# Kernel optimization log

Hardware: AMD Instinct MI355X
Metric: run time of the kernel (lower is better)

The kernel has to match this reference:

```python
import jax, jax.numpy as jnp
import numpy as np

JITTER = 1e-6
LOG_2PI_BASE = 2.0 * np.pi  # multiplied by sigma_sq inside log


def rbf_kernel(x1, x2, lengthscale, outputscale):
    """gpytorch ScaleKernel(RBFKernel): outputscale * exp(-0.5 * ||(x1-x2)/ls||^2)."""
    x1s = x1 / lengthscale
    x2s = x2 / lengthscale
    sq = (jnp.sum(x1s * x1s, axis=1)[:, None]
          + jnp.sum(x2s * x2s, axis=1)[None, :]
          - 2.0 * (x1s @ x2s.T))
    sq = jnp.maximum(sq, 0.0)
    return outputscale * jnp.exp(-0.5 * sq)


def setup_inputs() -> dict:
    key = jax.random.key(0)
    k = jax.random.split(key, 4)
    n, m, d = 8192, 512, 8
    return {
        "train_x": jax.random.normal(k[0], (n, d), dtype=jnp.float32),
        "train_y": jax.random.normal(k[1], (n,), dtype=jnp.float32),
        "inducing_points": jax.random.normal(k[2], (m, d), dtype=jnp.float32),
        "q_mu": jnp.zeros((m, 1), dtype=jnp.float32),
        "q_log_var": jnp.eye(m, dtype=jnp.float32),
        "likelihood_log_variance": jnp.asarray(0.0, dtype=jnp.float32),
        "lengthscale": jnp.asarray(1.0, dtype=jnp.float32),
        "outputscale": jnp.asarray(1.0, dtype=jnp.float32),
    }


def reference(train_x, train_y, inducing_points, q_mu, q_log_var,
              likelihood_log_variance, lengthscale, outputscale):
    n = train_x.shape[0]
    m = inducing_points.shape[0]
    eye_m = jnp.eye(m, dtype=train_x.dtype)

    # --- predict(train_x): q(f) = N(pred_mean, pred_cov) ---
    K_ff = rbf_kernel(train_x, train_x, lengthscale, outputscale)          # [n, n]
    K_uu = rbf_kernel(inducing_points, inducing_points, lengthscale, outputscale) + JITTER * eye_m
    K_uf = rbf_kernel(inducing_points, train_x, lengthscale, outputscale)  # [m, n]

    L_uu = jnp.linalg.cholesky(K_uu)                                       # lower [m, m]
    Lam = jax.scipy.linalg.solve_triangular(L_uu, K_uf, lower=True)        # [m, n]
    pred_mean = (Lam.T @ q_mu)[:, 0]                                       # [n]

    q_sqrt = jnp.tril(jnp.exp(0.5 * q_log_var))                            # [m, m]
    q_cov = q_sqrt @ q_sqrt.T + JITTER * eye_m                             # [m, m]

    S = K_ff - Lam.T @ Lam                                                 # [n, n]
    V = Lam.T @ q_cov                                                      # [n, m]
    pred_cov = S + V @ V.T                                                 # [n, n]

    # --- expected log likelihood E_{q(f)}[log N(y | f, sigma^2 I)] / n ---
    sigma_sq = jnp.exp(likelihood_log_variance)
    diff = train_y - pred_mean
    ell = jnp.sum(-0.5 * (diff * diff + jnp.diagonal(pred_cov)) / sigma_sq
                  - 0.5 * jnp.log(LOG_2PI_BASE * sigma_sq)) / n

    # --- KL( N(q_mu, q_cov) || N(0, I) ) / n ---
    Lq = jnp.linalg.cholesky(q_cov)
    logdet_q = 2.0 * jnp.sum(jnp.log(jnp.diagonal(Lq)))
    mu = q_mu[:, 0]
    kl = 0.5 * (jnp.trace(q_cov) + mu @ mu - m - logdet_q) / n

    return ell - kl
```

## Files before the change

### kernel.cpp

```cpp
#include <hip/hip_runtime.h>
#include <math.h>

#define MI 512
#define NPT 8192
#define JIT 1e-6f
#define LOG2PI 1.8378770664093453f

#define OFF_A     0
#define OFF_LINV  262144
#define OFF_QS    524288
#define OFF_QC    786432
#define OFF_DINV  1048576
#define OFF_PART  1081856
#define OFF_FLAGS 1082368
#define NFLAGS 209

#define FMA16(ACC,a0,a1,a2,a3,b0,b1,b2,b3) \
  ACC[0][0]+=a0*b0; ACC[0][1]+=a0*b1; ACC[0][2]+=a0*b2; ACC[0][3]+=a0*b3; \
  ACC[1][0]+=a1*b0; ACC[1][1]+=a1*b1; ACC[1][2]+=a1*b2; ACC[1][3]+=a1*b3; \
  ACC[2][0]+=a2*b0; ACC[2][1]+=a2*b1; ACC[2][2]+=a2*b2; ACC[2][3]+=a2*b3; \
  ACC[3][0]+=a3*b0; ACC[3][1]+=a3*b1; ACC[3][2]+=a3*b2; ACC[3][3]+=a3*b3;

__device__ __forceinline__ void wait_flag(unsigned* f, int tid) {
  if (tid == 0) {
    while (__hip_atomic_load(f, __ATOMIC_RELAXED, __HIP_MEMORY_SCOPE_AGENT) == 0)
      __builtin_amdgcn_s_sleep(2);
    __builtin_amdgcn_fence(__ATOMIC_ACQUIRE, "agent");
  }
  __syncthreads();
}
__device__ __forceinline__ void wait_count(unsigned* c, unsigned tgt, int tid) {
  if (tid == 0) {
    while (__hip_atomic_load(c, __ATOMIC_RELAXED, __HIP_MEMORY_SCOPE_AGENT) < tgt)
      __builtin_amdgcn_s_sleep(2);
    __builtin_amdgcn_fence(__ATOMIC_ACQUIRE, "agent");
  }
  __syncthreads();
}
__device__ __forceinline__ void raise_flag(unsigned* f, int tid) {
  __syncthreads();
  if (tid == 0) {
    __builtin_amdgcn_fence(__ATOMIC_RELEASE, "agent");
    __hip_atomic_store(f, 1u, __ATOMIC_RELAXED, __HIP_MEMORY_SCOPE_AGENT);
  }
}
__device__ __forceinline__ void publish_tile(unsigned* f, unsigned* cnt, int tid) {
  __syncthreads();
  if (tid == 0) {
    __builtin_amdgcn_fence(__ATOMIC_RELEASE, "agent");
    __hip_atomic_store(f, 1u, __ATOMIC_RELAXED, __HIP_MEMORY_SCOPE_AGENT);
    __hip_atomic_fetch_add(cnt, 1u, __ATOMIC_RELAXED, __HIP_MEMORY_SCOPE_AGENT);
  }
}

__global__ __launch_bounds__(256) void k_prep(const float* __restrict__ Z,
    const float* __restrict__ qlv, const float* __restrict__ lsP,
    const float* __restrict__ osP, float* __restrict__ ws) {
  int u = blockIdx.x*256 + threadIdx.x;
  if (blockIdx.x < 27) {
    int fi = blockIdx.x*256 + threadIdx.x;
    if (fi < NFLAGS*32) ((unsigned*)(ws + OFF_FLAGS))[fi] = 0u;
  }
  float ls = lsP[0], os = osP[0];
  float ils2 = 1.0f/(ls*ls);
  if (u < MI*MI) {
    int i = u >> 9, j = u & 511;
    float4 a0 = *(const float4*)(Z + i*8);
    float4 a1 = *(const float4*)(Z + i*8 + 4);
    float4 b0 = *(const float4*)(Z + j*8);
    float4 b1 = *(const float4*)(Z + j*8 + 4);
    float d0=a0.x-b0.x, d1=a0.y-b0.y, d2=a0.z-b0.z, d3=a0.w-b0.w;
    float d4=a1.x-b1.x, d5=a1.y-b1.y, d6=a1.z-b1.z, d7=a1.w-b1.w;
    float sq = d0*d0+d1*d1+d2*d2+d3*d3+d4*d4+d5*d5+d6*d6+d7*d7;
    float v = os*__expf(-0.5f*ils2*sq);
    if (i==j) v += JIT;
    ws[OFF_A + u] = v;
  } else {
    int w2 = u - MI*MI;
    if (w2 < MI*MI) {
      int i = w2 >> 9, j = w2 & 511;
      ws[OFF_QS + w2] = (j <= i) ? __expf(0.5f*qlv[w2]) : 0.0f;
    }
  }
}

__global__ __launch_bounds__(256) void k_gemm_nt(const float* __restrict__ X,
    const float* __restrict__ Y, float* __restrict__ O, float adiag) {
  __shared__ float Xs[64][20], Ys[64][20];
  int tid = threadIdx.x;
  int bi = blockIdx.y, bj = blockIdx.x;
  int ty4 = (tid >> 4)*4, tx4 = (tid & 15)*4;
  int lrow = tid >> 2, lc4 = (tid & 3)*4;
  float acc[4][4] = {{0.f}};
  for (int kc = 0; kc < 512; kc += 16) {
    float4 xa = *(const float4*)(X + (bi*64+lrow)*512 + kc + lc4);
    float4 ya = *(const float4*)(Y + (bj*64+lrow)*512 + kc + lc4);
    Xs[lrow][lc4+0]=xa.x; Xs[lrow][lc4+1]=xa.y; Xs[lrow][lc4+2]=xa.z; Xs[lrow][lc4+3]=xa.w;
    Ys[lrow][lc4+0]=ya.x; Ys[lrow][lc4+1]=ya.y; Ys[lrow][lc4+2]=ya.z; Ys[lrow][lc4+3]=ya.w;
    __syncthreads();
    #pragma unroll
    for (int kk = 0; kk < 16; ++kk) {
      float a0=Xs[ty4+0][kk],a1=Xs[ty4+1][kk],a2=Xs[ty4+2][kk],a3=Xs[ty4+3][kk];
      float b0=Ys[tx4+0][kk],b1=Ys[tx4+1][kk],b2=Ys[tx4+2][kk],b3=Ys[tx4+3][kk];
      FMA16(acc,a0,a1,a2,a3,b0,b1,b2,b3)
    }
    __syncthreads();
  }
  #pragma unroll
  for (int u = 0; u < 4; ++u)
    #pragma unroll
    for (int v = 0; v < 4; ++v) {
      int gi = bi*64+ty4+u, gj = bj*64+tx4+v;
      float o = acc[u][v]; if (gi==gj) o += adiag;
      O[gi*512+gj] = o;
    }
}

__global__ __launch_bounds__(256, 3) void k_dag(const float* __restrict__ X,
    const float* __restrict__ Yv, const float* __restrict__ Z,
    const float* __restrict__ qmu, const float* __restrict__ llvP,
    const float* __restrict__ lsP, const float* __restrict__ osP,
    float* __restrict__ ws) {
  __shared__ float SH[13340];
  float* A    = ws + OFF_A;
  float* LT   = ws + OFF_LINV;
  const float* QC = ws + OFF_QC;
  float* DINV = ws + OFF_DINV;
  float* PART = ws + OFF_PART;
  unsigned* FB = (unsigned*)(ws + OFF_FLAGS);
  #define FLA(i) (FB + (i)*32)
  int bid = blockIdx.x, tid = threadIdx.x;
  int ty4 = (tid >> 4)*4, tx4 = (tid & 15)*4;

  if (bid < 8) {
    __builtin_amdgcn_s_setprio(3);
    int b = bid, Rb = b*64;
    float* Dg = SH;
    float* Sa = SH + 4160;
    float* Sb = SH + 8320;
    float* TMP = SH + 12480;
    for (int e = tid; e < 4096; e += 256)
      Dg[(e>>6)*65 + (e&63)] = A[(Rb + (e>>6))*512 + Rb + (e&63)];

    for (int p = 0; p < b; ++p) {
      if (p > 0) wait_flag(FLA(144 + b*8 + p), tid);
      for (int e = tid; e < 4096; e += 256)
        Sb[(e>>6)*65 + (e&63)] = A[(Rb + (e>>6))*512 + p*64 + (e&63)];
      wait_flag(FLA(p), tid);
      for (int e = tid; e < 4096; e += 256)
        Sa[(e>>6)*65 + (e&63)] = DINV[p*4096 + e];
      __syncthreads();
      float acc2[4][4] = {{0.f}};
      for (int m = 0; m < 64; ++m) {
        float a0=Sb[(ty4+0)*65+m],a1=Sb[(ty4+1)*65+m],a2=Sb[(ty4+2)*65+m],a3=Sb[(ty4+3)*65+m];
        float b0=Sa[(tx4+0)*65+m],b1=Sa[(tx4+1)*65+m],b2=Sa[(tx4+2)*65+m],b3=Sa[(tx4+3)*65+m];
        FMA16(acc2,a0,a1,a2,a3,b0,b1,b2,b3)
      }
      __syncthreads();
      #pragma unroll
      for (int u = 0; u < 4; ++u)
        #pragma unroll
        for (int v = 0; v < 4; ++v) {
          Sb[(ty4+u)*65 + tx4+v] = acc2[u][v];
          A[(Rb+ty4+u)*512 + p*64 + tx4+v] = acc2[u][v];
        }
      raise_flag(FLA(8 + b*8 + p), tid);
      float c2[4][4] = {{0.f}};
      for (int m = 0; m < 64; ++m) {
        float a0=Sb[(ty4+0)*65+m],a1=Sb[(ty4+1)*65+m],a2=Sb[(ty4+2)*65+m],a3=Sb[(ty4+3)*65+m];
        float b0=Sb[(tx4+0)*65+m],b1=Sb[(tx4+1)*65+m],b2=Sb[(tx4+2)*65+m],b3=Sb[(tx4+3)*65+m];
        FMA16(c2,a0,a1,a2,a3,b0,b1,b2,b3)
      }
      #pragma unroll
      for (int u = 0; u < 4; ++u)
        #pragma unroll
        for (int v = 0; v < 4; ++v)
          Dg[(ty4+u)*65 + tx4+v] -= c2[u][v];
    }
    __syncthreads();

    for (int e = tid; e < 4096; e += 256) Sa[(e>>6)*65 + (e&63)] = 0.0f;
    __syncthreads();
    for (int t = 0; t < 4; ++t) {
      const int c0 = t*16;
      if (tid < 16) {
        float a[16];
        #pragma unroll
        for (int j = 0; j < 16; ++j) a[j] = Dg[(c0+tid)*65 + c0 + j];
        float rr = 0.f;
        #pragma unroll
        for (int j = 0; j < 16; ++j) {
          float d = __shfl(a[j], j);
          float r = rsqrtf(d);
          r = r*(1.5f - 0.5f*d*r*r);
          if (tid == j) rr = r;
          a[j] *= r;
          #pragma unroll
          for (int k = j+1; k < 16; ++k)
            a[k] -= a[j]*__shfl(a[j], k);
        }
        #pragma unroll
        for (int j = 0; j < 16; ++j)
          Dg[(c0+tid)*65 + c0 + j] = (j <= tid) ? a[j] : 0.0f;
        float v[16];
        #pragma unroll
        for (int i = 0; i < 16; ++i) {
          float s = (tid == i) ? 1.0f : 0.0f;
          #pragma unroll
          for (int k = 0; k < i; ++k)
            s -= Dg[(c0+i)*65 + c0 + k]*v[k];
          v[i] = s * __shfl(rr, i);
        }
        #pragma unroll
        for (int i = 0; i < 16; ++i)
          Sa[(c0+i)*65 + c0 + tid] = v[i];
      }
      __syncthreads();
      if (t < 3) {
        const int cnt = 48 - c0;
        const int r0 = c0 + 16;
        float res[3];
        int nout = cnt*16, idx = 0;
        for (int e = tid; e < nout; e += 256, ++idx) {
          int r = r0 + (e >> 4), j = e & 15;
          float s = 0.f;
          #pragma unroll
          for (int m = 0; m < 16; ++m)
            s += Dg[r*65 + c0 + m]*Sa[(c0+j)*65 + c0 + m];
          res[idx] = s;
        }
        __syncthreads();
        idx = 0;
        for (int e = tid; e < nout; e += 256, ++idx)
          Dg[(r0 + (e >> 4))*65 + c0 + (e & 15)] = res[idx];
        __syncthreads();
        for (int e = tid; e < cnt*cnt; e += 256) {
          int r = r0 + e/cnt, c = r0 + e%cnt;
          float s = 0.f;
          #pragma unroll
          for (int m = 0; m < 16; ++m)
            s += Dg[r*65 + c0 + m]*Dg[c*65 + c0 + m];
          Dg[r*65 + c] -= s;
        }
        __syncthreads();
      }
    }
    for (int d = 1; d < 4; ++d) {
      int nout = (4-d)*256;
      for (int e = tid; e < nout; e += 256) {
        int bs = e >> 8, I = bs, J = I + d;
        int i = (e >> 4) & 15, c = e & 15;
        float s = 0.f;
        for (int k = I; k < J; ++k) {
          #pragma unroll
          for (int m = 0; m < 16; ++m)
            s += Dg[(J*16+i)*65 + k*16+m]*Sa[(k*16+m)*65 + I*16+c];
        }
        TMP[bs*272 + i*17 + c] = s;
      }
      __syncthreads();
      for (int e = tid; e < nout; e += 256) {
        int bs = e >> 8, I = bs, J = I + d;
        int i = (e >> 4) & 15, c = e & 15;
        float s = 0.f;
        #pragma unroll
        for (int m = 0; m < 16; ++m)
          s += Sa[(J*16+i)*65 + J*16+m]*TMP[bs*272 + m*17 + c];
        Sa[(J*16+i)*65 + I*16+c] = -s;
      }
      __syncthreads();
    }
    for (int e = tid; e < 4096; e += 256)
      DINV[b*4096 + e] = Sa[(e>>6)*65 + (e&63)];
    raise_flag(FLA(b), tid);
    return;
  }

  if (bid < 44) {
    __builtin_amdgcn_s_setprio(2);
    int t = bid - 8;
    int s = 0, rem = t;
    while (rem >= s+1) { rem -= (s+1); ++s; }
    int J = rem;
    if (s == J) {
      wait_flag(FLA(s), tid);
      for (int e = tid; e < 4096; e += 256) {
        int i = e >> 6, j = e & 63;
        LT[(64*s+j)*512 + 64*s + i] = DINV[s*4096 + e];
      }
      publish_tile(FLA(72 + s*8 + J), FLA(136 + s), tid);
      return;
    }
    float* Ls = SH;
    float* Vs = SH + 4160;
    float* T  = SH + 8320;
    float acc[4][4] = {{0.f}};
    for (int k = J; k < s; ++k) {
      wait_flag(FLA(72 + k*8 + J), tid);
      wait_flag(FLA(8 + s*8 + k), tid);
      for (int e = tid; e < 1024; e += 256) {
        int row = e >> 4, m4 = (e & 15)*4;
        float4 a = *(const float4*)(A + (64*s+row)*512 + 64*k + m4);
        Ls[row*65+m4+0]=a.x; Ls[row*65+m4+1]=a.y; Ls[row*65+m4+2]=a.z; Ls[row*65+m4+3]=a.w;
        float4 v = *(const float4*)(LT + (64*J+row)*512 + 64*k + m4);
        Vs[(m4+0)*65+row]=v.x; Vs[(m4+1)*65+row]=v.y; Vs[(m4+2)*65+row]=v.z; Vs[(m4+3)*65+row]=v.w;
      }
      __syncthreads();
      for (int m = 0; m < 64; ++m) {
        float a0=Ls[(ty4+0)*65+m],a1=Ls[(ty4+1)*65+m],a2=Ls[(ty4+2)*65+m],a3=Ls[(ty4+3)*65+m];
        float b0=Vs[m*65+tx4+0],b1=Vs[m*65+tx4+1],b2=Vs[m*65+tx4+2],b3=Vs[m*65+tx4+3];
        FMA16(acc,a0,a1,a2,a3,b0,b1,b2,b3)
      }
      __syncthreads();
    }
    wait_flag(FLA(s), tid);
    #pragma unroll
    for (int u = 0; u < 4; ++u)
      #pragma unroll
      for (int v = 0; v < 4; ++v)
        T[(ty4+u)*65 + tx4+v] = acc[u][v];
    for (int e = tid; e < 4096; e += 256) Ls[(e>>6)*65 + (e&63)] = DINV[s*4096 + e];
    __syncthreads();
    float acc2[4][4] = {{0.f}};
    for (int m = 0; m < 64; ++m) {
      float a0=Ls[(ty4+0)*65+m],a1=Ls[(ty4+1)*65+m],a2=Ls[(ty4+2)*65+m],a3=Ls[(ty4+3)*65+m];
      float b0=T[m*65+tx4+0],b1=T[m*65+tx4+1],b2=T[m*65+tx4+2],b3=T[m*65+tx4+3];
      FMA16(acc2,a0,a1,a2,a3,b0,b1,b2,b3)
    }
    #pragma unroll
    for (int u = 0; u < 4; ++u)
      #pragma unroll
      for (int v = 0; v < 4; ++v)
        LT[(64*J+tx4+v)*512 + 64*s+ty4+u] = -acc2[u][v];
    publish_tile(FLA(72 + s*8 + J), FLA(136 + s), tid);
    return;
  }

  if (bid < 65) {
    __builtin_amdgcn_s_setprio(2);
    int hid = bid - 44;
    int b = 2, rem = hid;
    while (rem >= b-1) { rem -= (b-1); ++b; }
    int p = rem + 1;
    float* Sa = SH;
    float* Sb = SH + 4160;
    float gacc[4][4] = {{0.f}};
    for (int pp = 0; pp < p; ++pp) {
      wait_flag(FLA(8 + b*8 + pp), tid);
      wait_flag(FLA(8 + p*8 + pp), tid);
      for (int e = tid; e < 4096; e += 256) {
        int row = e>>6, col = e&63;
        Sa[row*65+col] = A[(b*64+row)*512 + pp*64 + col];
        Sb[row*65+col] = A[(p*64+row)*512 + pp*64 + col];
      }
      __syncthreads();
      for (int m = 0; m < 64; ++m) {
        float a0=Sa[(ty4+0)*65+m],a1=Sa[(ty4+1)*65+m],a2=Sa[(ty4+2)*65+m],a3=Sa[(ty4+3)*65+m];
        float b0=Sb[(tx4+0)*65+m],b1=Sb[(tx4+1)*65+m],b2=Sb[(tx4+2)*65+m],b3=Sb[(tx4+3)*65+m];
        FMA16(gacc,a0,a1,a2,a3,b0,b1,b2,b3)
      }
      __syncthreads();
    }
    #pragma unroll
    for (int u = 0; u < 4; ++u)
      #pragma unroll
      for (int v = 0; v < 4; ++v)
        A[(b*64+ty4+u)*512 + p*64 + tx4+v] -= gacc[u][v];
    raise_flag(FLA(144 + b*8 + p), tid);
    return;
  }

  {
    int B = bid - 65;
    float* KL  = SH;
    float* PB  = SH + 8192;
    float* FB2 = SH + 11456;
    float* qsh = SH + 12736;
    float* Xs  = SH + 8192;
    float* RD  = SH + 8192;
    float* elli= SH + 9824;
    float ls = lsP[0], os = osP[0], llv = llvP[0];
    float ils2 = 1.0f/(ls*ls);
    if (tid < 128) { int pp = tid>>3, d = tid&7; Xs[pp*8+d] = X[(B*16+pp)*8 + d]; }
    qsh[tid] = qmu[tid]; qsh[tid+256] = qmu[tid+256];
    __syncthreads();
    for (int e = tid; e < 8192; e += 256) {
      int cc = e >> 4, pp = e & 15;
      float4 z0 = *(const float4*)(Z + cc*8);
      float4 z1 = *(const float4*)(Z + cc*8 + 4);
      float d0=z0.x-Xs[pp*8+0], d1=z0.y-Xs[pp*8+1], d2=z0.z-Xs[pp*8+2], d3=z0.w-Xs[pp*8+3];
      float d4=z1.x-Xs[pp*8+4], d5=z1.y-Xs[pp*8+5], d6=z1.z-Xs[pp*8+6], d7=z1.w-Xs[pp*8+7];
      float sq = d0*d0+d1*d1+d2*d2+d3*d3+d4*d4+d5*d5+d6*d6+d7*d7;
      KL[e] = os*__expf(-0.5f*ils2*sq);
    }

    int gq = tid >> 6;
    int lr = (tid >> 2) & 15;
    int lrow4 = lr*4;
    int pq4 = (tid & 3)*4;
    int rq4 = (tid >> 2)*4;
    float pmp[4] = {0.f,0.f,0.f,0.f}, lsp[4] = {0.f,0.f,0.f,0.f};
    float ua0[4][4] = {{0.f}}, ua1[4][4] = {{0.f}};

    for (int s = 0; s < 8; ++s) {
      wait_count(FLA(136 + s), (unsigned)(s+1), tid);
      int Q = 16*(s+1);
      int cbeg = gq*Q, cend = cbeg + Q;
      float acc[4][4] = {{0.f}};
      const float* Lcol = LT + 64*s + lrow4;
      #pragma unroll 4
      for (int c = cbeg; c < cend; ++c) {
        float4 kv = *(const float4*)&KL[c*16 + pq4];
        float4 lv = *(const float4*)(Lcol + c*512);
        FMA16(acc, lv.x,lv.y,lv.z,lv.w, kv.x,kv.y,kv.z,kv.w)
      }
      if (gq > 0) {
        float* pb = PB + (gq-1)*1088;
        #pragma unroll
        for (int u = 0; u < 4; ++u)
          #pragma unroll
          for (int v = 0; v < 4; ++v)
            pb[(lrow4+u)*17 + pq4+v] = acc[u][v];
      }
      __syncthreads();
      if (gq == 0) {
        #pragma unroll
        for (int u = 0; u < 4; ++u) {
          float qv = qsh[64*s + lrow4 + u];
          #pragma unroll
          for (int v = 0; v < 4; ++v) {
            float f = acc[u][v]
                    + PB[(lrow4+u)*17 + pq4+v]
                    + PB[1088 + (lrow4+u)*17 + pq4+v]
                    + PB[2176 + (lrow4+u)*17 + pq4+v];
            FB2[(lrow4+u)*20 + pq4+v] = f;
            pmp[v] += f*qv;
            lsp[v] += f*f;
          }
        }
      }
      __syncthreads();
      #pragma unroll 2
      for (int cl = 0; cl < 64; ++cl) {
        float4 kv = *(const float4*)&FB2[cl*20 + pq4];
        float4 q0 = *(const float4*)(QC + (64*s+cl)*512 + rq4);
        float4 q1 = *(const float4*)(QC + (64*s+cl)*512 + 256 + rq4);
        FMA16(ua0, q0.x,q0.y,q0.z,q0.w, kv.x,kv.y,kv.z,kv.w)
        FMA16(ua1, q1.x,q1.y,q1.z,q1.w, kv.x,kv.y,kv.z,kv.w)
      }
    }
    __syncthreads();

    if (gq == 0) {
      #pragma unroll
      for (int v = 0; v < 4; ++v) {
        RD[lr*17 + pq4+v] = pmp[v];
        RD[272 + lr*17 + pq4+v] = lsp[v];
      }
    }
    float usq[4] = {0.f,0.f,0.f,0.f};
    #pragma unroll
    for (int u = 0; u < 4; ++u)
      #pragma unroll
      for (int v = 0; v < 4; ++v)
        usq[v] += ua0[u][v]*ua0[u][v] + ua1[u][v]*ua1[u][v];
    #pragma unroll
    for (int v = 0; v < 4; ++v)
      RD[544 + (tid>>2)*17 + pq4+v] = usq[v];
    __syncthreads();
    if (tid < 16) {
      float pm = 0.f, lq = 0.f, us = 0.f;
      for (int r2 = 0; r2 < 16; ++r2) {
        pm += RD[r2*17 + tid];
        lq += RD[272 + r2*17 + tid];
      }
      for (int r2 = 0; r2 < 64; ++r2)
        us += RD[544 + r2*17 + tid];
      int gi = B*16 + tid;
      float diff = Yv[gi] - pm;
      float diagc = os + us - lq;
      float iss = __expf(-llv);
      elli[tid] = -0.5f*((diff*diff + diagc)*iss + (LOG2PI + llv));
    }
    __syncthreads();
    if (tid == 0) {
      float sum = 0.f;
      #pragma unroll
      for (int i2 = 0; i2 < 16; ++i2) sum += elli[i2];
      PART[B] = sum;
    }
  }
}

__global__ __launch_bounds__(256) void k_final(const float* __restrict__ qmu,
    const float* __restrict__ qlv, float* __restrict__ ws, float* __restrict__ out) {
  __shared__ double sh[256];
  int tid = threadIdx.x;
  const float* QC = ws + OFF_QC;
  const float* PART = ws + OFF_PART;
  double pa = 0.0, tr = 0.0, mm = 0.0, ld = 0.0;
  for (int i = tid; i < 512; i += 256) {
    pa += (double)PART[i];
    tr += (double)QC[i*513];
    double q = (double)qmu[i]; mm += q*q;
    ld += (double)qlv[i*513];
  }
  double vals[4] = {pa, tr, mm, ld};
  double res[4];
  for (int t2 = 0; t2 < 4; ++t2) {
    sh[tid] = vals[t2]; __syncthreads();
    for (int s2 = 128; s2 > 0; s2 >>= 1) {
      if (tid < s2) sh[tid] += sh[tid+s2];
      __syncthreads();
    }
    res[t2] = sh[0]; __syncthreads();
  }
  if (tid == 0) {
    double n = 8192.0;
    double ell = res[0]/n;
    double kl = 0.5*(res[1] + res[2] - 512.0 - res[3])/n;
    out[0] = (float)(ell - kl);
  }
}

extern "C" void kernel_launch(void* const* d_in, const int* in_sizes, int n_in,
                              void* d_out, int out_size, void* d_ws, size_t ws_size,
                              hipStream_t stream) {
  (void)in_sizes; (void)n_in; (void)out_size; (void)ws_size;
  const float* X   = (const float*)d_in[0];
  const float* Y   = (const float*)d_in[1];
  const float* Z   = (const float*)d_in[2];
  const float* qmu = (const float*)d_in[3];
  const float* qlv = (const float*)d_in[4];
  const float* llv = (const float*)d_in[5];
  const float* ls  = (const float*)d_in[6];
  const float* os  = (const float*)d_in[7];
  float* ws = (float*)d_ws;
  float* out = (float*)d_out;

  k_prep<<<2048, 256, 0, stream>>>(Z, qlv, ls, os, ws);
  k_gemm_nt<<<dim3(8,8), 256, 0, stream>>>(ws+OFF_QS, ws+OFF_QS, ws+OFF_QC, JIT);
  k_dag<<<577, 256, 0, stream>>>(X, Y, Z, qmu, llv, ls, os, ws);
  k_final<<<1, 256, 0, stream>>>(qmu, qlv, ws, out);
}
```

Measured before the change: 394.5 us.

## Restructure blocked Cholesky DAG into single diagonal worker with atomic SYRK accumulation

New measurement: 466.1 us. +18.2%, slower.

```diff
diff --git a/kernel.cpp b/kernel.cpp
--- a/kernel.cpp
+++ b/kernel.cpp
@@ -60,6 +60,8 @@
   if (blockIdx.x < 27) {
     int fi = blockIdx.x*256 + threadIdx.x;
     if (fi < NFLAGS*32) ((unsigned*)(ws + OFF_FLAGS))[fi] = 0u;
+  } else if (blockIdx.x < 155) {
+    ws[OFF_DINV + (blockIdx.x-27)*256 + threadIdx.x] = 0.0f;
   }
   float ls = lsP[0], os = osP[0];
   float ils2 = 1.0f/(ls*ls);
@@ -132,153 +134,262 @@
   int bid = blockIdx.x, tid = threadIdx.x;
   int ty4 = (tid >> 4)*4, tx4 = (tid & 15)*4;
 
-  if (bid < 8) {
+  if (bid == 0) {
     __builtin_amdgcn_s_setprio(3);
-    int b = bid, Rb = b*64;
-    float* Dg = SH;
-    float* Sa = SH + 4160;
-    float* Sb = SH + 8320;
-    float* TMP = SH + 12480;
+    float* Dg   = SH;
+    float* Dinv = SH + 4160;
+    float* Gs   = SH + 8320;
+    float* TMP  = SH + 8320;
+
+    for (int b = 0; b < 8; ++b) {
+      if (b > 0) {
+        if (b >= 2) wait_flag(FLA(144 + b), tid);
+        if (b >= 2) wait_count(FLA(152 + b), (unsigned)(b-1), tid);
+        for (int e = tid; e < 4096; e += 256)
+          Gs[(e>>6)*65 + (e&63)] = A[(b*64 + (e>>6))*512 + (b-1)*64 + (e&63)];
+        __syncthreads();
+        float acc2[4][4] = {{0.f}};
+        for (int m = 0; m < 64; ++m) {
+          float a0=Gs[(ty4+0)*65+m],a1=Gs[(ty4+1)*65+m],a2=Gs[(ty4+2)*65+m],a3=Gs[(ty4+3)*65+m];
+          float b0=Dinv[(tx4+0)*65+m],b1=Dinv[(tx4+1)*65+m],b2=Dinv[(tx4+2)*65+m],b3=Dinv[(tx4+3)*65+m];
+          FMA16(acc2,a0,a1,a2,a3,b0,b1,b2,b3)
+        }
+        __syncthreads();
+        #pragma unroll
+        for (int u = 0; u < 4; ++u)
+          #pragma unroll
+          for (int v = 0; v < 4; ++v) {
+            Gs[(ty4+u)*65 + tx4+v] = acc2[u][v];
+            A[(b*64+ty4+u)*512 + (b-1)*64 + tx4+v] = acc2[u][v];
+          }
+        for (int e = tid; e < 4096; e += 256) {
+          float d = A[(b*64 + (e>>6))*512 + b*64 + (e&63)];
+          if (b >= 2) d -= DINV[b*4096 + e];
+          Dg[(e>>6)*65 + (e&63)] = d;
+        }
+        raise_flag(FLA(8 + b*8 + (b-1)), tid);
+        float c2[4][4] = {{0.f}};
+        for (int m = 0; m < 64; ++m) {
+          float a0=Gs[(ty4+0)*65+m],a1=Gs[(ty4+1)*65+m],a2=Gs[(ty4+2)*65+m],a3=Gs[(ty4+3)*65+m];
+          float b0=Gs[(tx4+0)*65+m],b1=Gs[(tx4+1)*65+m],b2=Gs[(tx4+2)*65+m],b3=Gs[(tx4+3)*65+m];
+          FMA16(c2,a0,a1,a2,a3,b0,b1,b2,b3)
+        }
+        #pragma unroll
+        for (int u = 0; u < 4; ++u)
+          #pragma unroll
+          for (int v = 0; v < 4; ++v)
+            Dg[(ty4+u)*65 + tx4+v] -= c2[u][v];
+        __syncthreads();
+      } else {
+        for (int e = tid; e < 4096; e += 256)
+          Dg[(e>>6)*65 + (e&63)] = A[(e>>6)*512 + (e&63)];
+        __syncthreads();
+      }
+
+      for (int e = tid; e < 4096; e += 256) Dinv[(e>>6)*65 + (e&63)] = 0.0f;
+      __syncthreads();
+      for (int t = 0; t < 4; ++t) {
+        const int c0 = t*16;
+        if (tid < 16) {
+          float a[16];
+          #pragma unroll
+          for (int j = 0; j < 16; ++j) a[j] = Dg[(c0+tid)*65 + c0 + j];
+          float rr = 0.f;
+          #pragma unroll
+          for (int j = 0; j < 16; ++j) {
+            float d = __shfl(a[j], j);
+            float r = rsqrtf(d);
+            r = r*(1.5f - 0.5f*d*r*r);
+            if (tid == j) rr = r;
+            a[j] *= r;
+            #pragma unroll
+            for (int k = j+1; k < 16; ++k)
+              a[k] -= a[j]*__shfl(a[j], k);
+          }
+          #pragma unroll
+          for (int j = 0; j < 16; ++j)
+            Dg[(c0+tid)*65 + c0 + j] = (j <= tid) ? a[j] : 0.0f;
+          float v[16];
+          #pragma unroll
+          for (int i = 0; i < 16; ++i) {
+            float s = (tid == i) ? 1.0f : 0.0f;
+            #pragma unroll
+            for (int k = 0; k < i; ++k)
+              s -= Dg[(c0+i)*65 + c0 + k]*v[k];
+            v[i] = s * __shfl(rr, i);
+          }
+          #pragma unroll
+          for (int i = 0; i < 16; ++i)
+            Dinv[(c0+i)*65 + c0 + tid] = v[i];
+        }
+        __syncthreads();
+        if (t < 3) {
+          const int cnt = 48 - c0;
+          const int r0 = c0 + 16;
+          float res[3];
+          int nout = cnt*16, idx = 0;
+          for (int e = tid; e < nout; e += 256, ++idx) {
+            int r = r0 + (e >> 4), j = e & 15;
+            float s = 0.f;
+            #pragma unroll
+            for (int m = 0; m < 16; ++m)
+              s += Dg[r*65 + c0 + m]*Dinv[(c0+j)*65 + c0 + m];
+            res[idx] = s;
+          }
+          __syncthreads();
+          idx = 0;
+          for (int e = tid; e < nout; e += 256, ++idx)
+            Dg[(r0 + (e >> 4))*65 + c0 + (e & 15)] = res[idx];
+          __syncthreads();
+          for (int e = tid; e < cnt*cnt; e += 256) {
+            int r = r0 + e/cnt, c = r0 + e%cnt;
+            float s = 0.f;
+            #pragma unroll
+            for (int m = 0; m < 16; ++m)
+              s += Dg[r*65 + c0 + m]*Dg[c*65 + c0 + m];
+            Dg[r*65 + c] -= s;
+          }
+          __syncthreads();
+        }
+      }
+      for (int d = 1; d < 4; ++d) {
+        int nout = (4-d)*256;
+        for (int e = tid; e < nout; e += 256) {
+          int bs = e >> 8, I = bs, J = I + d;
+          int i = (e >> 4) & 15, c = e & 15;
+          float s = 0.f;
+          for (int k = I; k < J; ++k) {
+            #pragma unroll
+            for (int m = 0; m < 16; ++m)
+              s += Dg[(J*16+i)*65 + k*16+m]*Dinv[(k*16+m)*65 + I*16+c];
+          }
+          TMP[bs*272 + i*17 + c] = s;
+        }
+        __syncthreads();
+        for (int e = tid; e < nout; e += 256) {
+          int bs = e >> 8, I = bs, J = I + d;
+          int i = (e >> 4) & 15, c = e & 15;
+          float s = 0.f;
+          #pragma unroll
+          for (int m = 0; m < 16; ++m)
+            s += Dinv[(J*16+i)*65 + J*16+m]*TMP[bs*272 + m*17 + c];
+          Dinv[(J*16+i)*65 + I*16+c] = -s;
+        }
+        __syncthreads();
+      }
+      for (int e = tid; e < 4096; e += 256)
+        DINV[b*4096 + e] = Dinv[(e>>6)*65 + (e&63)];
+      raise_flag(FLA(b), tid);
+      __syncthreads();
+    }
+    return;
+  }
+
+  if (bid < 22) {
+    __builtin_amdgcn_s_setprio(2);
+    int hid = bid - 1;
+    int p = 0, rem = hid;
+    while (rem >= 6 - p) { rem -= (6 - p); ++p; }
+    int b = p + 2 + rem;
+    float* Sa = SH;
+    float* Sb = SH + 4160;
+    float* T  = SH + 8320;
+    float gacc[4][4] = {{0.f}};
+    for (int pp = 0; pp < p; ++pp) {
+      wait_flag(FLA(8 + b*8 + pp), tid);
+      wait_flag(FLA(8 + p*8 + pp), tid);
+      for (int e = tid; e < 4096; e += 256) {
+        int row = e>>6, col = e&63;
+        Sa[row*65+col] = A[(b*64+row)*512 + pp*64 + col];
+        Sb[row*65+col] = A[(p*64+row)*512 + pp*64 + col];
+      }
+      __syncthreads();
+      for (int m = 0; m < 64; ++m) {
+        float a0=Sa[(ty4+0)*65+m],a1=Sa[(ty4+1)*65+m],a2=Sa[(ty4+2)*65+m],a3=Sa[(ty4+3)*65+m];
+        float b0=Sb[(tx4+0)*65+m],b1=Sb[(tx4+1)*65+m],b2=Sb[(tx4+2)*65+m],b3=Sb[(tx4+3)*65+m];
+        FMA16(gacc,a0,a1,a2,a3,b0,b1,b2,b3)
+      }
+      __syncthreads();
+    }
+    wait_flag(FLA(p), tid);
+    #pragma unroll
+    for (int u = 0; u < 4; ++u)
+      #pragma unroll
+      for (int v = 0; v < 4; ++v)
+        T[(ty4+u)*65 + tx4+v] = A[(b*64+ty4+u)*512 + p*64 + tx4+v] - gacc[u][v];
     for (int e = tid; e < 4096; e += 256)
-      Dg[(e>>6)*65 + (e&63)] = A[(Rb + (e>>6))*512 + Rb + (e&63)];
-
-    for (int p = 0; p < b; ++p) {
-      if (p > 0) wait_flag(FLA(144 + b*8 + p), tid);
-      for (int e = tid; e < 4096; e += 256)
-        Sb[(e>>6)*65 + (e&63)] = A[(Rb + (e>>6))*512 + p*64 + (e&63)];
-      wait_flag(FLA(p), tid);
-      for (int e = tid; e < 4096; e += 256)
-        Sa[(e>>6)*65 + (e&63)] = DINV[p*4096 + e];
-      __syncthreads();
-      float acc2[4][4] = {{0.f}};
+      Sa[(e>>6)*65 + (e&63)] = DINV[p*4096 + e];
+    __syncthreads();
+    float acc2[4][4] = {{0.f}};
+    for (int m = 0; m < 64; ++m) {
+      float a0=T[(ty4+0)*65+m],a1=T[(ty4+1)*65+m],a2=T[(ty4+2)*65+m],a3=T[(ty4+3)*65+m];
+      float b0=Sa[(tx4+0)*65+m],b1=Sa[(tx4+1)*65+m],b2=Sa[(tx4+2)*65+m],b3=Sa[(tx4+3)*65+m];
+      FMA16(acc2,a0,a1,a2,a3,b0,b1,b2,b3)
+    }
+    __syncthreads();
+    #pragma unroll
+    for (int u = 0; u < 4; ++u)
+      #pragma unroll
+      for (int v = 0; v < 4; ++v) {
+        Sb[(ty4+u)*65 + tx4+v] = acc2[u][v];
+        A[(b*64+ty4+u)*512 + p*64 + tx4+v] = acc2[u][v];
+      }
+    raise_flag(FLA(8 + b*8 + p), tid);
+    float c2[4][4] = {{0.f}};
+    for (int m = 0; m < 64; ++m) {
+      float a0=Sb[(ty4+0)*65+m],a1=Sb[(ty4+1)*65+m],a2=Sb[(ty4+2)*65+m],a3=Sb[(ty4+3)*65+m];
+      float b0=Sb[(tx4+0)*65+m],b1=Sb[(tx4+1)*65+m],b2=Sb[(tx4+2)*65+m],b3=Sb[(tx4+3)*65+m];
+      FMA16(c2,a0,a1,a2,a3,b0,b1,b2,b3)
+    }
+    #pragma unroll
+    for (int u = 0; u < 4; ++u)
+      #pragma unroll
+      for (int v = 0; v < 4; ++v)
+        __hip_atomic_fetch_add(&DINV[b*4096 + (ty4+u)*64 + tx4+v], c2[u][v],
+                               __ATOMIC_RELAXED, __HIP_MEMORY_SCOPE_AGENT);
+    __syncthreads();
+    if (tid == 0) {
+      __builtin_amdgcn_fence(__ATOMIC_RELEASE, "agent");
+      __hip_atomic_fetch_add(FLA(152 + b), 1u, __ATOMIC_RELAXED, __HIP_MEMORY_SCOPE_AGENT);
+    }
+    return;
+  }
+
+  if (bid < 28) {
+    __builtin_amdgcn_s_setprio(2);
+    int b = bid - 22 + 2;
+    int p = b - 1;
+    float* Sa = SH;
+    float* Sb = SH + 4160;
+    float gacc[4][4] = {{0.f}};
+    for (int pp = 0; pp < p; ++pp) {
+      wait_flag(FLA(8 + b*8 + pp), tid);
+      wait_flag(FLA(8 + p*8 + pp), tid);
+      for (int e = tid; e < 4096; e += 256) {
+        int row = e>>6, col = e&63;
+        Sa[row*65+col] = A[(b*64+row)*512 + pp*64 + col];
+        Sb[row*65+col] = A[(p*64+row)*512 + pp*64 + col];
+      }
+      __syncthreads();
       for (int m = 0; m < 64; ++m) {
-        float a0=Sb[(ty4+0)*65+m],a1=Sb[(ty4+1)*65+m],a2=Sb[(ty4+2)*65+m],a3=Sb[(ty4+3)*65+m];
-        float b0=Sa[(tx4+0)*65+m],b1=Sa[(tx4+1)*65+m],b2=Sa[(tx4+2)*65+m],b3=Sa[(tx4+3)*65+m];
-        FMA16(acc2,a0,a1,a2,a3,b0,b1,b2,b3)
-      }
-      __syncthreads();
-      #pragma unroll
-      for (int u = 0; u < 4; ++u)
-        #pragma unroll
-        for (int v = 0; v < 4; ++v) {
-          Sb[(ty4+u)*65 + tx4+v] = acc2[u][v];
-          A[(Rb+ty4+u)*512 + p*64 + tx4+v] = acc2[u][v];
-        }
-      raise_flag(FLA(8 + b*8 + p), tid);
-      float c2[4][4] = {{0.f}};
-      for (int m = 0; m < 64; ++m) {
-        float a0=Sb[(ty4+0)*65+m],a1=Sb[(ty4+1)*65+m],a2=Sb[(ty4+2)*65+m],a3=Sb[(ty4+3)*65+m];
+        float a0=Sa[(ty4+0)*65+m],a1=Sa[(ty4+1)*65+m],a2=Sa[(ty4+2)*65+m],a3=Sa[(ty4+3)*65+m];
         float b0=Sb[(tx4+0)*65+m],b1=Sb[(tx4+1)*65+m],b2=Sb[(tx4+2)*65+m],b3=Sb[(tx4+3)*65+m];
-        FMA16(c2,a0,a1,a2,a3,b0,b1,b2,b3)
-      }
-      #pragma unroll
-      for (int u = 0; u < 4; ++u)
-        #pragma unroll
-        for (int v = 0; v < 4; ++v)
-          Dg[(ty4+u)*65 + tx4+v] -= c2[u][v];
-    }
-    __syncthreads();
-
-    for (int e = tid; e < 4096; e += 256) Sa[(e>>6)*65 + (e&63)] = 0.0f;
-    __syncthreads();
-    for (int t = 0; t < 4; ++t) {
-      const int c0 = t*16;
-      if (tid < 16) {
-        float a[16];
-        #pragma unroll
-        for (int j = 0; j < 16; ++j) a[j] = Dg[(c0+tid)*65 + c0 + j];
-        float rr = 0.f;
-        #pragma unroll
-        for (int j = 0; j < 16; ++j) {
-          float d = __shfl(a[j], j);
-          float r = rsqrtf(d);
-          r = r*(1.5f - 0.5f*d*r*r);
-          if (tid == j) rr = r;
-          a[j] *= r;
-          #pragma unroll
-          for (int k = j+1; k < 16; ++k)
-            a[k] -= a[j]*__shfl(a[j], k);
-        }
-        #pragma unroll
-        for (int j = 0; j < 16; ++j)
-          Dg[(c0+tid)*65 + c0 + j] = (j <= tid) ? a[j] : 0.0f;
-        float v[16];
-        #pragma unroll
-        for (int i = 0; i < 16; ++i) {
-          float s = (tid == i) ? 1.0f : 0.0f;
-          #pragma unroll
-          for (int k = 0; k < i; ++k)
-            s -= Dg[(c0+i)*65 + c0 + k]*v[k];
-          v[i] = s * __shfl(rr, i);
-        }
-        #pragma unroll
-        for (int i = 0; i < 16; ++i)
-          Sa[(c0+i)*65 + c0 + tid] = v[i];
-      }
-      __syncthreads();
-      if (t < 3) {
-        const int cnt = 48 - c0;
-        const int r0 = c0 + 16;
-        float res[3];
-        int nout = cnt*16, idx = 0;
-        for (int e = tid; e < nout; e += 256, ++idx) {
-          int r = r0 + (e >> 4), j = e & 15;
-          float s = 0.f;
-          #pragma unroll
-          for (int m = 0; m < 16; ++m)
-            s += Dg[r*65 + c0 + m]*Sa[(c0+j)*65 + c0 + m];
-          res[idx] = s;
-        }
-        __syncthreads();
-        idx = 0;
-        for (int e = tid; e < nout; e += 256, ++idx)
-          Dg[(r0 + (e >> 4))*65 + c0 + (e & 15)] = res[idx];
-        __syncthreads();
-        for (int e = tid; e < cnt*cnt; e += 256) {
-          int r = r0 + e/cnt, c = r0 + e%cnt;
-          float s = 0.f;
-          #pragma unroll
-          for (int m = 0; m < 16; ++m)
-            s += Dg[r*65 + c0 + m]*Dg[c*65 + c0 + m];
-          Dg[r*65 + c] -= s;
-        }
-        __syncthreads();
-      }
-    }
-    for (int d = 1; d < 4; ++d) {
-      int nout = (4-d)*256;
-      for (int e = tid; e < nout; e += 256) {
-        int bs = e >> 8, I = bs, J = I + d;
-        int i = (e >> 4) & 15, c = e & 15;
-        float s = 0.f;
-        for (int k = I; k < J; ++k) {
-          #pragma unroll
-          for (int m = 0; m < 16; ++m)
-            s += Dg[(J*16+i)*65 + k*16+m]*Sa[(k*16+m)*65 + I*16+c];
-        }
-        TMP[bs*272 + i*17 + c] = s;
-      }
-      __syncthreads();
-      for (int e = tid; e < nout; e += 256) {
-        int bs = e >> 8, I = bs, J = I + d;
-        int i = (e >> 4) & 15, c = e & 15;
-        float s = 0.f;
-        #pragma unroll
-        for (int m = 0; m < 16; ++m)
-          s += Sa[(J*16+i)*65 + J*16+m]*TMP[bs*272 + m*17 + c];
-        Sa[(J*16+i)*65 + I*16+c] = -s;
-      }
-      __syncthreads();
-    }
-    for (int e = tid; e < 4096; e += 256)
-      DINV[b*4096 + e] = Sa[(e>>6)*65 + (e&63)];
-    raise_flag(FLA(b), tid);
+        FMA16(gacc,a0,a1,a2,a3,b0,b1,b2,b3)
+      }
+      __syncthreads();
+    }
+    #pragma unroll
+    for (int u = 0; u < 4; ++u)
+      #pragma unroll
+      for (int v = 0; v < 4; ++v)
+        A[(b*64+ty4+u)*512 + p*64 + tx4+v] -= gacc[u][v];
+    raise_flag(FLA(144 + b), tid);
     return;
   }
 
-  if (bid < 44) {
+  if (bid < 64) {
     __builtin_amdgcn_s_setprio(2);
-    int t = bid - 8;
+    int t = bid - 28;
     int s = 0, rem = t;
     while (rem >= s+1) { rem -= (s+1); ++s; }
     int J = rem;
@@ -336,42 +447,8 @@
     return;
   }
 
-  if (bid < 65) {
-    __builtin_amdgcn_s_setprio(2);
-    int hid = bid - 44;
-    int b = 2, rem = hid;
-    while (rem >= b-1) { rem -= (b-1); ++b; }
-    int p = rem + 1;
-    float* Sa = SH;
-    float* Sb = SH + 4160;
-    float gacc[4][4] = {{0.f}};
-    for (int pp = 0; pp < p; ++pp) {
-      wait_flag(FLA(8 + b*8 + pp), tid);
-      wait_flag(FLA(8 + p*8 + pp), tid);
-      for (int e = tid; e < 4096; e += 256) {
-        int row = e>>6, col = e&63;
-        Sa[row*65+col] = A[(b*64+row)*512 + pp*64 + col];
-        Sb[row*65+col] = A[(p*64+row)*512 + pp*64 + col];
-      }
-      __syncthreads();
-      for (int m = 0; m < 64; ++m) {
-        float a0=Sa[(ty4+0)*65+m],a1=Sa[(ty4+1)*65+m],a2=Sa[(ty4+2)*65+m],a3=Sa[(ty4+3)*65+m];
-        float b0=Sb[(tx4+0)*65+m],b1=Sb[(tx4+1)*65+m],b2=Sb[(tx4+2)*65+m],b3=Sb[(tx4+3)*65+m];
-        FMA16(gacc,a0,a1,a2,a3,b0,b1,b2,b3)
-      }
-      __syncthreads();
-    }
-    #pragma unroll
-    for (int u = 0; u < 4; ++u)
-      #pragma unroll
-      for (int v = 0; v < 4; ++v)
-        A[(b*64+ty4+u)*512 + p*64 + tx4+v] -= gacc[u][v];
-    raise_flag(FLA(144 + b*8 + p), tid);
-    return;
-  }
-
   {
-    int B = bid - 65;
+    int B = bid - 64;
     float* KL  = SH;
     float* PB  = SH + 8192;
     float* FB2 = SH + 11456;
@@ -540,6 +617,6 @@
 
   k_prep<<<2048, 256, 0, stream>>>(Z, qlv, ls, os, ws);
   k_gemm_nt<<<dim3(8,8), 256, 0, stream>>>(ws+OFF_QS, ws+OFF_QS, ws+OFF_QC, JIT);
-  k_dag<<<577, 256, 0, stream>>>(X, Y, Z, qmu, llv, ls, os, ws);
+  k_dag<<<576, 256, 0, stream>>>(X, Y, Z, qmu, llv, ls, os, ws);
   k_final<<<1, 256, 0, stream>>>(qmu, qlv, ws, out);
 }
```

## Fold q_cov GEMM and final reduction into the persistent DAG kernel

Applied to the files above, without the earlier changes.

Result: faster. 359.0 us (-9.0%).

```diff
diff --git a/kernel.cpp b/kernel.cpp
--- a/kernel.cpp
+++ b/kernel.cpp
@@ -13,7 +13,7 @@
 #define OFF_DINV  1048576
 #define OFF_PART  1081856
 #define OFF_FLAGS 1082368
-#define NFLAGS 209
+#define NFLAGS 211
 
 #define FMA16(ACC,a0,a1,a2,a3,b0,b1,b2,b3) \
   ACC[0][0]+=a0*b0; ACC[0][1]+=a0*b1; ACC[0][2]+=a0*b2; ACC[0][3]+=a0*b3; \
@@ -84,43 +84,12 @@
   }
 }
 
-__global__ __launch_bounds__(256) void k_gemm_nt(const float* __restrict__ X,
-    const float* __restrict__ Y, float* __restrict__ O, float adiag) {
-  __shared__ float Xs[64][20], Ys[64][20];
-  int tid = threadIdx.x;
-  int bi = blockIdx.y, bj = blockIdx.x;
-  int ty4 = (tid >> 4)*4, tx4 = (tid & 15)*4;
-  int lrow = tid >> 2, lc4 = (tid & 3)*4;
-  float acc[4][4] = {{0.f}};
-  for (int kc = 0; kc < 512; kc += 16) {
-    float4 xa = *(const float4*)(X + (bi*64+lrow)*512 + kc + lc4);
-    float4 ya = *(const float4*)(Y + (bj*64+lrow)*512 + kc + lc4);
-    Xs[lrow][lc4+0]=xa.x; Xs[lrow][lc4+1]=xa.y; Xs[lrow][lc4+2]=xa.z; Xs[lrow][lc4+3]=xa.w;
-    Ys[lrow][lc4+0]=ya.x; Ys[lrow][lc4+1]=ya.y; Ys[lrow][lc4+2]=ya.z; Ys[lrow][lc4+3]=ya.w;
-    __syncthreads();
-    #pragma unroll
-    for (int kk = 0; kk < 16; ++kk) {
-      float a0=Xs[ty4+0][kk],a1=Xs[ty4+1][kk],a2=Xs[ty4+2][kk],a3=Xs[ty4+3][kk];
-      float b0=Ys[tx4+0][kk],b1=Ys[tx4+1][kk],b2=Ys[tx4+2][kk],b3=Ys[tx4+3][kk];
-      FMA16(acc,a0,a1,a2,a3,b0,b1,b2,b3)
-    }
-    __syncthreads();
-  }
-  #pragma unroll
-  for (int u = 0; u < 4; ++u)
-    #pragma unroll
-    for (int v = 0; v < 4; ++v) {
-      int gi = bi*64+ty4+u, gj = bj*64+tx4+v;
-      float o = acc[u][v]; if (gi==gj) o += adiag;
-      O[gi*512+gj] = o;
-    }
-}
-
 __global__ __launch_bounds__(256, 3) void k_dag(const float* __restrict__ X,
     const float* __restrict__ Yv, const float* __restrict__ Z,
-    const float* __restrict__ qmu, const float* __restrict__ llvP,
-    const float* __restrict__ lsP, const float* __restrict__ osP,
-    float* __restrict__ ws) {
+    const float* __restrict__ qmu, const float* __restrict__ qlv,
+    const float* __restrict__ llvP, const float* __restrict__ lsP,
+    const float* __restrict__ osP, float* __restrict__ ws,
+    float* __restrict__ out) {
   __shared__ float SH[13340];
   float* A    = ws + OFF_A;
   float* LT   = ws + OFF_LINV;
@@ -370,8 +339,48 @@
     return;
   }
 
+  if (bid < 129) {
+    __builtin_amdgcn_s_setprio(1);
+    int cid = bid - 65;
+    int bi = cid >> 3, bj = cid & 7;
+    const float* QSp = ws + OFF_QS;
+    float* QCw = ws + OFF_QC;
+    float* Xs2 = SH;
+    float* Ys2 = SH + 1280;
+    int lrow = tid >> 2, lc4 = (tid & 3)*4;
+    float acc[4][4] = {{0.f}};
+    for (int kc = 0; kc < 512; kc += 16) {
+      float4 xa = *(const float4*)(QSp + (bi*64+lrow)*512 + kc + lc4);
+      float4 ya = *(const float4*)(QSp + (bj*64+lrow)*512 + kc + lc4);
+      Xs2[lrow*20+lc4+0]=xa.x; Xs2[lrow*20+lc4+1]=xa.y; Xs2[lrow*20+lc4+2]=xa.z; Xs2[lrow*20+lc4+3]=xa.w;
+      Ys2[lrow*20+lc4+0]=ya.x; Ys2[lrow*20+lc4+1]=ya.y; Ys2[lrow*20+lc4+2]=ya.z; Ys2[lrow*20+lc4+3]=ya.w;
+      __syncthreads();
+      #pragma unroll
+      for (int kk = 0; kk < 16; ++kk) {
+        float a0=Xs2[(ty4+0)*20+kk],a1=Xs2[(ty4+1)*20+kk],a2=Xs2[(ty4+2)*20+kk],a3=Xs2[(ty4+3)*20+kk];
+        float b0=Ys2[(tx4+0)*20+kk],b1=Ys2[(tx4+1)*20+kk],b2=Ys2[(tx4+2)*20+kk],b3=Ys2[(tx4+3)*20+kk];
+        FMA16(acc,a0,a1,a2,a3,b0,b1,b2,b3)
+      }
+      __syncthreads();
+    }
+    #pragma unroll
+    for (int u = 0; u < 4; ++u)
+      #pragma unroll
+      for (int v = 0; v < 4; ++v) {
+        int gi = bi*64+ty4+u, gj = bj*64+tx4+v;
+        float o = acc[u][v]; if (gi==gj) o += JIT;
+        QCw[gi*512+gj] = o;
+      }
+    __syncthreads();
+    if (tid == 0) {
+      __builtin_amdgcn_fence(__ATOMIC_RELEASE, "agent");
+      __hip_atomic_fetch_add(FLA(208), 1u, __ATOMIC_RELAXED, __HIP_MEMORY_SCOPE_AGENT);
+    }
+    return;
+  }
+
   {
-    int B = bid - 65;
+    int B = bid - 129;
     float* KL  = SH;
     float* PB  = SH + 8192;
     float* FB2 = SH + 11456;
@@ -379,6 +388,7 @@
     float* Xs  = SH + 8192;
     float* RD  = SH + 8192;
     float* elli= SH + 9824;
+    int* lastf = (int*)(SH + 13248);
     float ls = lsP[0], os = osP[0], llv = llvP[0];
     float ils2 = 1.0f/(ls*ls);
     if (tid < 128) { int pp = tid>>3, d = tid&7; Xs[pp*8+d] = X[(B*16+pp)*8 + d]; }
@@ -393,6 +403,7 @@
       float sq = d0*d0+d1*d1+d2*d2+d3*d3+d4*d4+d5*d5+d6*d6+d7*d7;
       KL[e] = os*__expf(-0.5f*ils2*sq);
     }
+    wait_count(FLA(208), 64u, tid);
 
     int gq = tid >> 6;
     int lr = (tid >> 2) & 15;
@@ -488,38 +499,39 @@
       #pragma unroll
       for (int i2 = 0; i2 < 16; ++i2) sum += elli[i2];
       PART[B] = sum;
-    }
-  }
-}
-
-__global__ __launch_bounds__(256) void k_final(const float* __restrict__ qmu,
-    const float* __restrict__ qlv, float* __restrict__ ws, float* __restrict__ out) {
-  __shared__ double sh[256];
-  int tid = threadIdx.x;
-  const float* QC = ws + OFF_QC;
-  const float* PART = ws + OFF_PART;
-  double pa = 0.0, tr = 0.0, mm = 0.0, ld = 0.0;
-  for (int i = tid; i < 512; i += 256) {
-    pa += (double)PART[i];
-    tr += (double)QC[i*513];
-    double q = (double)qmu[i]; mm += q*q;
-    ld += (double)qlv[i*513];
-  }
-  double vals[4] = {pa, tr, mm, ld};
-  double res[4];
-  for (int t2 = 0; t2 < 4; ++t2) {
-    sh[tid] = vals[t2]; __syncthreads();
-    for (int s2 = 128; s2 > 0; s2 >>= 1) {
-      if (tid < s2) sh[tid] += sh[tid+s2];
-      __syncthreads();
-    }
-    res[t2] = sh[0]; __syncthreads();
-  }
-  if (tid == 0) {
-    double n = 8192.0;
-    double ell = res[0]/n;
-    double kl = 0.5*(res[1] + res[2] - 512.0 - res[3])/n;
-    out[0] = (float)(ell - kl);
+      __builtin_amdgcn_fence(__ATOMIC_RELEASE, "agent");
+      unsigned old = __hip_atomic_fetch_add(FLA(209), 1u, __ATOMIC_RELAXED, __HIP_MEMORY_SCOPE_AGENT);
+      lastf[0] = (old == 511u) ? 1 : 0;
+    }
+    __syncthreads();
+    if (lastf[0]) {
+      if (tid == 0) __builtin_amdgcn_fence(__ATOMIC_ACQUIRE, "agent");
+      __syncthreads();
+      double* sh = (double*)SH;
+      double pa = 0.0, tr = 0.0, mm = 0.0, ld = 0.0;
+      for (int i = tid; i < 512; i += 256) {
+        pa += (double)PART[i];
+        tr += (double)QC[i*513];
+        double q = (double)qmu[i]; mm += q*q;
+        ld += (double)qlv[i*513];
+      }
+      double vals[4] = {pa, tr, mm, ld};
+      double res[4];
+      for (int t2 = 0; t2 < 4; ++t2) {
+        sh[tid] = vals[t2]; __syncthreads();
+        for (int s2 = 128; s2 > 0; s2 >>= 1) {
+          if (tid < s2) sh[tid] += sh[tid+s2];
+          __syncthreads();
+        }
+        res[t2] = sh[0]; __syncthreads();
+      }
+      if (tid == 0) {
+        double n = 8192.0;
+        double ell = res[0]/n;
+        double kl = 0.5*(res[1] + res[2] - 512.0 - res[3])/n;
+        out[0] = (float)(ell - kl);
+      }
+    }
   }
 }
 
@@ -539,7 +551,5 @@
   float* out = (float*)d_out;
 
   k_prep<<<2048, 256, 0, stream>>>(Z, qlv, ls, os, ws);
-  k_gemm_nt<<<dim3(8,8), 256, 0, stream>>>(ws+OFF_QS, ws+OFF_QS, ws+OFF_QC, JIT);
-  k_dag<<<577, 256, 0, stream>>>(X, Y, Z, qmu, llv, ls, os, ws);
-  k_final<<<1, 256, 0, stream>>>(qmu, qlv, ws, out);
-}
+  k_dag<<<641, 256, 0, stream>>>(X, Y, Z, qmu, qlv, llv, ls, os, ws, out);
+}
```
